# Optimization experiments

Measured on AMD Instinct MI355X. Metric: run time of the kernel, lower is better.

## Reference

```python
import jax, jax.numpy as jnp
import numpy as np


def _conv(x, w, b):
    # PyTorch Conv2d(k=4, s=2, p=1): NCHW x OIHW correlation
    y = jax.lax.conv_general_dilated(x, w, window_strides=(2, 2),
                                     padding=((1, 1), (1, 1)),
                                     dimension_numbers=('NCHW', 'OIHW', 'NCHW'))
    return y + b[None, :, None, None]


def _conv_t(x, w, b):
    # PyTorch ConvTranspose2d(k=4, s=2, p=1); w has torch shape (Cin, Cout, 4, 4).
    # Adjoint of strided correlation = correlation with spatially-flipped,
    # channel-swapped kernel and lhs dilation; pad = k - 1 - p = 2.
    wk = jnp.flip(w, (2, 3)).transpose(1, 0, 2, 3)  # (Cout, Cin, 4, 4)
    y = jax.lax.conv_general_dilated(x, wk, window_strides=(1, 1),
                                     padding=((2, 2), (2, 2)),
                                     lhs_dilation=(2, 2),
                                     dimension_numbers=('NCHW', 'OIHW', 'NCHW'))
    return y + b[None, :, None, None]


def setup_inputs() -> dict:
    key = jax.random.key(0)
    ks = jax.random.split(key, 18)
    s = 0.05
    inp = {'x': jax.random.normal(ks[0], (32, 3, 256, 256), jnp.float32)}
    # encoder weights (OIHW)
    enc_shapes = [(64, 3, 4, 4), (128, 64, 4, 4), (256, 128, 4, 4), (512, 256, 4, 4)]
    for i, sh in enumerate(enc_shapes):
        inp[f'e_w{i+1}'] = jax.random.normal(ks[1 + i], sh, jnp.float32) * s
        inp[f'e_b{i+1}'] = jnp.zeros((sh[0],), jnp.float32)
    # decoder weights (torch ConvTranspose2d layout: Cin, Cout, kH, kW)
    dec_shapes = [(512, 128, 4, 4), (128, 64, 4, 4), (64, 32, 4, 4), (32, 3, 4, 4)]
    for i, sh in enumerate(dec_shapes):
        inp[f'd_w{i+1}'] = jax.random.normal(ks[5 + i], sh, jnp.float32) * s
        inp[f'd_b{i+1}'] = jnp.zeros((sh[1],), jnp.float32)
    # codebook (num_embeddings=1024, embedding_dim=512)
    inp['embed'] = jax.random.normal(ks[9], (1024, 512), jnp.float32)
    return inp


def reference(x, e_w1, e_b1, e_w2, e_b2, e_w3, e_b3, e_w4, e_b4,
              d_w1, d_b1, d_w2, d_b2, d_w3, d_b3, d_w4, d_b4, embed):
    # encoder
    h = jax.nn.relu(_conv(x, e_w1, e_b1))
    h = jax.nn.relu(_conv(h, e_w2, e_b2))
    h = jax.nn.relu(_conv(h, e_w3, e_b3))
    z = jax.nn.relu(_conv(h, e_w4, e_b4))  # (B, 512, 16, 16)
    # quantizer: NCHW -> NHWC -> flat (B*H*W, D)
    B, D, H, W = z.shape
    z_flat = z.transpose(0, 2, 3, 1).reshape(-1, D)
    # squared L2 distance to each code: ||z||^2 - 2 z.E^T + ||E||^2
    dist = (jnp.sum(z_flat ** 2, axis=1, keepdims=True)
            - 2.0 * z_flat @ embed.T
            + jnp.sum(embed ** 2, axis=1))  # (N, K)
    idx = jnp.argmin(dist, axis=1)
    quantized = embed[idx]  # gather == one_hot @ embed
    z_q = quantized.reshape(B, H, W, D).transpose(0, 3, 1, 2)  # NCHW
    # decoder
    h = jax.nn.relu(_conv_t(z_q, d_w1, d_b1))
    h = jax.nn.relu(_conv_t(h, d_w2, d_b2))
    h = jax.nn.relu(_conv_t(h, d_w3, d_b3))
    out = jnp.tanh(_conv_t(h, d_w4, d_b4))  # (B, 3, 256, 256)
    return out
```

## Files before the change

kernel.cpp:

```cpp
#include <hip/hip_runtime.h>
#include <math.h>


typedef __attribute__((ext_vector_type(8))) short bf16x8;
typedef __attribute__((ext_vector_type(4))) float f32x4;
union FragU { unsigned u[4]; bf16x8 v; };

__device__ __forceinline__ unsigned bf16_rne(unsigned u) {
    return (u + 0x7FFFu + ((u >> 16) & 1u)) >> 16;
}
__device__ __forceinline__ unsigned pack_split(float v) {
    unsigned u = __builtin_bit_cast(unsigned, v);
    unsigned hi = bf16_rne(u);
    float hif = __builtin_bit_cast(float, hi << 16);
    float r = v - hif;
    unsigned lo = bf16_rne(__builtin_bit_cast(unsigned, r));
    return hi | (lo << 16);
}

__global__ void __launch_bounds__(256) pack_tensor(
    const float* __restrict__ s, unsigned* __restrict__ d, int n)
{
    int i = blockIdx.x * 256 + threadIdx.x;
    if (i < n) d[i] = pack_split(s[i]);
}

__global__ void __launch_bounds__(256) pack_w1(
    const float* __restrict__ w, unsigned* __restrict__ wq)
{
    int idx = blockIdx.x * 256 + threadIdx.x;
    if (idx >= 64 * 64) return;
    int k = idx & 63, oc = idx >> 6;
    float v = (k < 48) ? w[oc * 48 + k] : 0.0f;
    wq[idx] = pack_split(v);
}

template<int Cin, int Cout>
__global__ void __launch_bounds__(256) repack_wt(
    const float* __restrict__ w, unsigned* __restrict__ wq)
{
    constexpr int TOT = 16 * Cin * Cout;
    int idx = blockIdx.x * 256 + threadIdx.x;
    if (idx >= TOT) return;
    int t  = idx & 3;
    int ci = (idx >> 2) % Cin;
    int rest = (idx >> 2) / Cin;
    int co  = rest % Cout;
    int par = rest / Cout;
    int dy = par >> 1, dx = par & 1;
    int r = t >> 1, s = t & 1;
    int ky = 3 - dy - 2 * r;
    int kx = 3 - dx - 2 * s;
    float v = w[(((size_t)ci * Cout + co) * 4 + ky) * 4 + kx];
    wq[idx] = pack_split(v);
}

__global__ void __launch_bounds__(256) embed_transpose(
    const float* __restrict__ embed, float* __restrict__ et)
{
    int idx = blockIdx.x * 256 + threadIdx.x;
    int c = idx & 1023, k = idx >> 10;
    et[idx] = embed[(size_t)c * 512 + k];
}

template<int Cin, int H, int W, int Cout, int NB, int PACKO>
__global__ void __launch_bounds__(256) conv4s2_mfma(
    const unsigned* __restrict__ xp, const unsigned* __restrict__ wp,
    const float* __restrict__ bias, float* __restrict__ y)
{
    constexpr int OH = H / 2, OW = W / 2;
    constexpr int LOG_OW = (OW == 64) ? 6 : (OW == 32) ? 5 : 4;
    constexpr int R   = 64 / OW;
    constexpr int RT  = 2 * R + 2;
    constexpr int CS  = W + 2;
    constexpr int XEL = 2 * RT * CS;
    constexpr int XIT = (XEL + 255) / 256;
    constexpr int K   = Cin * 16;
    constexpr int NC  = Cin / 2;
    constexpr int NT  = NB / 64;
    constexpr int WIT = NB / 8;
    constexpr int MBC = 32 * OH * OW / 64;
    constexpr int XPAD = (XEL + 7) & ~7;
    constexpr int SM1 = XPAD + NB * 36;
    constexpr int SM2 = NB * 68;
    constexpr int SMEM = SM1 > SM2 ? SM1 : SM2;

    __shared__ unsigned smem[SMEM];
    unsigned* raw = smem;
    unsigned* wb  = smem + XPAD;

    int bid = blockIdx.x;
    int mb = bid % MBC, ng = bid / MBC;
    int oc0 = ng * NB;
    int m0 = mb * 64;
    int nimg = m0 / (OH * OW);
    int sp0 = m0 % (OH * OW);
    int oyb = sp0 >> LOG_OW;

    int tid  = threadIdx.x;
    int lane = tid & 63, wv = tid >> 6;
    int lm = lane & 15, q = lane >> 4;
    int n0w = wv * 16 * NT;

    const unsigned* xbase = xp + (size_t)nimg * Cin * H * W;

    int  goff[XIT];
    bool gok[XIT];
#pragma unroll
    for (int s = 0; s < XIT; ++s) {
        int i = tid + 256 * s;
        goff[s] = 0; gok[s] = false;
        if (i < XEL) {
            int lc = i % CS;
            int t2 = i / CS;
            int lr = t2 % RT;
            int c  = t2 / RT;
            int gr = 2 * oyb - 1 + lr;
            int gc = lc - 1;
            bool ok = ((unsigned)gr < (unsigned)H) && ((unsigned)gc < (unsigned)W);
            goff[s] = ok ? (c * H * W + gr * W + gc) : 0;
            gok[s]  = ok;
        }
    }
    const unsigned* wbase = wp + (size_t)(oc0 + (tid >> 5)) * K + (tid & 31);
    int wlds0 = (tid >> 5) * 36 + (tid & 31);

    f32x4 acc[4][NT];
#pragma unroll
    for (int nt = 0; nt < NT; ++nt) {
        float b = bias[oc0 + n0w + nt * 16 + lm];
#pragma unroll
        for (int mt = 0; mt < 4; ++mt)
#pragma unroll
            for (int r = 0; r < 4; ++r) acc[mt][nt][r] = b;
    }

    unsigned pfa[XIT];
    unsigned pfb[WIT];

    auto load_chunk = [&](int ch) {
        const unsigned* cb = xbase + (size_t)(ch * 2) * (H * W);
#pragma unroll
        for (int s = 0; s < XIT; ++s) {
            unsigned v = 0;
            if (gok[s]) v = cb[goff[s]];
            pfa[s] = v;
        }
        const unsigned* wc = wbase + ch * 32;
#pragma unroll
        for (int s = 0; s < WIT; ++s) pfb[s] = wc[(size_t)s * 8 * K];
    };
    auto store_chunk = [&]() {
#pragma unroll
        for (int s = 0; s < XIT; ++s) {
            int i = tid + 256 * s;
            if (i < XEL) raw[i] = pfa[s];
        }
#pragma unroll
        for (int s = 0; s < WIT; ++s) wb[wlds0 + s * 288] = pfb[s];
    };

    load_chunk(0);
#pragma unroll 1
    for (int ch = 0; ch < NC; ++ch) {
        __syncthreads();
        store_chunk();
        __syncthreads();
        if (ch + 1 < NC) load_chunk(ch + 1);

        FragU bhi[NT], blo[NT];
#pragma unroll
        for (int nt = 0; nt < NT; ++nt) {
            const unsigned* bp = &wb[(n0w + nt * 16 + lm) * 36 + q * 8];
            uint4 p0 = *(const uint4*)bp;
            uint4 p1 = *(const uint4*)(bp + 4);
            unsigned e0 = p0.x, e1 = p0.y, e2 = p0.z, e3 = p0.w;
            unsigned e4 = p1.x, e5 = p1.y, e6 = p1.z, e7 = p1.w;
            bhi[nt].u[0] = (e0 & 0xffffu) | (e1 << 16);
            bhi[nt].u[1] = (e2 & 0xffffu) | (e3 << 16);
            bhi[nt].u[2] = (e4 & 0xffffu) | (e5 << 16);
            bhi[nt].u[3] = (e6 & 0xffffu) | (e7 << 16);
            blo[nt].u[0] = (e0 >> 16) | (e1 & 0xffff0000u);
            blo[nt].u[1] = (e2 >> 16) | (e3 & 0xffff0000u);
            blo[nt].u[2] = (e4 >> 16) | (e5 & 0xffff0000u);
            blo[nt].u[3] = (e6 >> 16) | (e7 & 0xffff0000u);
        }
#pragma unroll
        for (int mt = 0; mt < 4; ++mt) {
            int m = mt * 16 + lm;
            int oyl = m >> LOG_OW, oxl = m & (OW - 1);
            int c = q >> 1, rb = 2 * oyl + (q & 1) * 2;
            const unsigned* rp = &raw[(c * RT + rb) * CS + 2 * oxl];
            uint2 a0 = *(const uint2*)rp;
            uint2 a1 = *(const uint2*)(rp + 2);
            uint2 a2 = *(const uint2*)(rp + CS);
            uint2 a3 = *(const uint2*)(rp + CS + 2);
            FragU ahi, alo;
            ahi.u[0] = (a0.x & 0xffffu) | (a0.y << 16);
            ahi.u[1] = (a1.x & 0xffffu) | (a1.y << 16);
            ahi.u[2] = (a2.x & 0xffffu) | (a2.y << 16);
            ahi.u[3] = (a3.x & 0xffffu) | (a3.y << 16);
            alo.u[0] = (a0.x >> 16) | (a0.y & 0xffff0000u);
            alo.u[1] = (a1.x >> 16) | (a1.y & 0xffff0000u);
            alo.u[2] = (a2.x >> 16) | (a2.y & 0xffff0000u);
            alo.u[3] = (a3.x >> 16) | (a3.y & 0xffff0000u);
#pragma unroll
            for (int nt = 0; nt < NT; ++nt) {
                acc[mt][nt] = __builtin_amdgcn_mfma_f32_16x16x32_bf16(
                    ahi.v, bhi[nt].v, acc[mt][nt], 0, 0, 0);
                acc[mt][nt] = __builtin_amdgcn_mfma_f32_16x16x32_bf16(
                    ahi.v, blo[nt].v, acc[mt][nt], 0, 0, 0);
                acc[mt][nt] = __builtin_amdgcn_mfma_f32_16x16x32_bf16(
                    alo.v, bhi[nt].v, acc[mt][nt], 0, 0, 0);
            }
        }
    }

    __syncthreads();
    float* cs = (float*)smem;
#pragma unroll
    for (int mt = 0; mt < 4; ++mt)
#pragma unroll
        for (int nt = 0; nt < NT; ++nt) {
            int nl = n0w + nt * 16 + lm;
#pragma unroll
            for (int r = 0; r < 4; ++r)
                cs[nl * 68 + mt * 16 + q * 4 + r] = acc[mt][nt][r];
        }
    __syncthreads();
    {
        constexpr int QT = 256 / NB;
        constexpr int MQ = 64 / QT;
        int nl = tid / QT, qt = tid % QT;
        size_t gb = ((size_t)(nimg * Cout + oc0 + nl)) * (OH * OW) + sp0 + qt * MQ;
#pragma unroll
        for (int i2 = 0; i2 < MQ / 4; ++i2) {
            float4 v = *(float4*)&cs[nl * 68 + qt * MQ + 4 * i2];
            v.x = fmaxf(v.x, 0.0f); v.y = fmaxf(v.y, 0.0f);
            v.z = fmaxf(v.z, 0.0f); v.w = fmaxf(v.w, 0.0f);
            if (PACKO) {
                uint4 p;
                p.x = pack_split(v.x); p.y = pack_split(v.y);
                p.z = pack_split(v.z); p.w = pack_split(v.w);
                *(uint4*)((unsigned*)y + gb + 4 * i2) = p;
            } else {
                *(float4*)(y + gb + 4 * i2) = v;
            }
        }
    }
}

template<int Cin, int CINR, int H, int W, int Cout, int MT, int NT, int PACKO>
__global__ void __launch_bounds__(256) conv4s2_mfma_g(
    const unsigned* __restrict__ xp, const unsigned* __restrict__ wp,
    const float* __restrict__ bias, float* __restrict__ y)
{
    constexpr int OH = H / 2, OW = W / 2;
    constexpr int OWB = (OW >= 64) ? 64 : OW;
    constexpr int LOG_OWB = (OWB == 64) ? 6 : (OWB == 32) ? 5 : 4;
    constexpr int LOG_OW  = (OW == 128) ? 7 : (OW == 64) ? 6 : (OW == 32) ? 5 : 4;
    constexpr int R   = 64 / OWB;
    constexpr int RT  = 2 * R + 2;
    constexpr int CS  = 2 * OWB + 2;
    constexpr int XEL = 2 * RT * CS;
    constexpr int XIT = (XEL + 255) / 256;
    constexpr int K   = Cin * 16;
    constexpr int NC  = Cin / 2;
    constexpr int NB  = Cout;
    constexpr int WIT = NB / 8;
    constexpr int WN  = Cout / (16 * NT);
    constexpr int WM  = 4 / WN;
    static_assert(WM * MT * 16 == 64, "M tiling");
    static_assert(WN * NT * 16 == Cout, "N tiling");
    constexpr int MBC = 32 * OH * OW / 64;
    constexpr int XPAD = (XEL + 7) & ~7;
    constexpr int SM1 = XPAD + NB * 36;
    constexpr int SM2 = NB * 68;
    constexpr int SMEM = SM1 > SM2 ? SM1 : SM2;

    __shared__ unsigned smem[SMEM];
    unsigned* raw = smem;
    unsigned* wb  = smem + XPAD;

    int bid = blockIdx.x;
    int mb = bid % MBC, ng = bid / MBC;
    int oc0 = ng * NB;
    int m0 = bid % MBC * 64;
    m0 = mb * 64;
    int nimg = m0 / (OH * OW);
    int sp0 = m0 % (OH * OW);
    int oyb = sp0 >> LOG_OW;
    int oxb = sp0 & (OW - 1);

    int tid  = threadIdx.x;
    int lane = tid & 63, wv = tid >> 6;
    int lm = lane & 15, q = lane >> 4;
    int wm = wv / WN, wn = wv % WN;

    const unsigned* xbase = xp + (size_t)nimg * CINR * H * W;

    int  goff[XIT];
    bool gok[XIT];
    int  cidx[XIT];
#pragma unroll
    for (int s = 0; s < XIT; ++s) {
        int i = tid + 256 * s;
        goff[s] = 0; gok[s] = false; cidx[s] = 0;
        if (i < XEL) {
            int lc = i % CS;
            int t2 = i / CS;
            int lr = t2 % RT;
            int c  = t2 / RT;
            int gr = 2 * oyb - 1 + lr;
            int gc = 2 * oxb - 1 + lc;
            bool ok = ((unsigned)gr < (unsigned)H) && ((unsigned)gc < (unsigned)W);
            goff[s] = ok ? (c * H * W + gr * W + gc) : 0;
            gok[s]  = ok;
            cidx[s] = c;
        }
    }
    const unsigned* wbase = wp + (size_t)(oc0 + (tid >> 5)) * K + (tid & 31);
    int wlds0 = (tid >> 5) * 36 + (tid & 31);

    f32x4 acc[MT][NT];
#pragma unroll
    for (int nt = 0; nt < NT; ++nt) {
        float b = bias[oc0 + wn * NT * 16 + nt * 16 + lm];
#pragma unroll
        for (int mt = 0; mt < MT; ++mt)
#pragma unroll
            for (int r = 0; r < 4; ++r) acc[mt][nt][r] = b;
    }

    unsigned pfa[XIT];
    unsigned pfb[WIT];

    auto load_chunk = [&](int ch) {
        const unsigned* cb = xbase + (size_t)(ch * 2) * (H * W);
#pragma unroll
        for (int s = 0; s < XIT; ++s) {
            unsigned v = 0;
            bool okc = (2 * ch + cidx[s]) < CINR;
            if (gok[s] && okc) v = cb[goff[s]];
            pfa[s] = v;
        }
        const unsigned* wc = wbase + ch * 32;
#pragma unroll
        for (int s = 0; s < WIT; ++s) pfb[s] = wc[(size_t)s * 8 * K];
    };
    auto store_chunk = [&]() {
#pragma unroll
        for (int s = 0; s < XIT; ++s) {
            int i = tid + 256 * s;
            if (i < XEL) raw[i] = pfa[s];
        }
#pragma unroll
        for (int s = 0; s < WIT; ++s) wb[wlds0 + s * 288] = pfb[s];
    };

    load_chunk(0);
#pragma unroll 1
    for (int ch = 0; ch < NC; ++ch) {
        __syncthreads();
        store_chunk();
        __syncthreads();
        if (ch + 1 < NC) load_chunk(ch + 1);

        FragU bhi[NT], blo[NT];
#pragma unroll
        for (int nt = 0; nt < NT; ++nt) {
            const unsigned* bp = &wb[(wn * NT * 16 + nt * 16 + lm) * 36 + q * 8];
            uint4 p0 = *(const uint4*)bp;
            uint4 p1 = *(const uint4*)(bp + 4);
            unsigned e0 = p0.x, e1 = p0.y, e2 = p0.z, e3 = p0.w;
            unsigned e4 = p1.x, e5 = p1.y, e6 = p1.z, e7 = p1.w;
            bhi[nt].u[0] = (e0 & 0xffffu) | (e1 << 16);
            bhi[nt].u[1] = (e2 & 0xffffu) | (e3 << 16);
            bhi[nt].u[2] = (e4 & 0xffffu) | (e5 << 16);
            bhi[nt].u[3] = (e6 & 0xffffu) | (e7 << 16);
            blo[nt].u[0] = (e0 >> 16) | (e1 & 0xffff0000u);
            blo[nt].u[1] = (e2 >> 16) | (e3 & 0xffff0000u);
            blo[nt].u[2] = (e4 >> 16) | (e5 & 0xffff0000u);
            blo[nt].u[3] = (e6 >> 16) | (e7 & 0xffff0000u);
        }
#pragma unroll
        for (int mt = 0; mt < MT; ++mt) {
            int m = wm * (MT * 16) + mt * 16 + lm;
            int oyl = m >> LOG_OWB, oxl = m & (OWB - 1);
            int c = q >> 1, rb = 2 * oyl + (q & 1) * 2;
            const unsigned* rp = &raw[(c * RT + rb) * CS + 2 * oxl];
            uint2 a0 = *(const uint2*)rp;
            uint2 a1 = *(const uint2*)(rp + 2);
            uint2 a2 = *(const uint2*)(rp + CS);
            uint2 a3 = *(const uint2*)(rp + CS + 2);
            FragU ahi, alo;
            ahi.u[0] = (a0.x & 0xffffu) | (a0.y << 16);
            ahi.u[1] = (a1.x & 0xffffu) | (a1.y << 16);
            ahi.u[2] = (a2.x & 0xffffu) | (a2.y << 16);
            ahi.u[3] = (a3.x & 0xffffu) | (a3.y << 16);
            alo.u[0] = (a0.x >> 16) | (a0.y & 0xffff0000u);
            alo.u[1] = (a1.x >> 16) | (a1.y & 0xffff0000u);
            alo.u[2] = (a2.x >> 16) | (a2.y & 0xffff0000u);
            alo.u[3] = (a3.x >> 16) | (a3.y & 0xffff0000u);
#pragma unroll
            for (int nt = 0; nt < NT; ++nt) {
                acc[mt][nt] = __builtin_amdgcn_mfma_f32_16x16x32_bf16(
                    ahi.v, bhi[nt].v, acc[mt][nt], 0, 0, 0);
                acc[mt][nt] = __builtin_amdgcn_mfma_f32_16x16x32_bf16(
                    ahi.v, blo[nt].v, acc[mt][nt], 0, 0, 0);
                acc[mt][nt] = __builtin_amdgcn_mfma_f32_16x16x32_bf16(
                    alo.v, bhi[nt].v, acc[mt][nt], 0, 0, 0);
            }
        }
    }

    __syncthreads();
    float* cs = (float*)smem;
#pragma unroll
    for (int mt = 0; mt < MT; ++mt)
#pragma unroll
        for (int nt = 0; nt < NT; ++nt) {
            int nl  = wn * NT * 16 + nt * 16 + lm;
            int mb2 = wm * (MT * 16) + mt * 16 + q * 4;
#pragma unroll
            for (int r = 0; r < 4; ++r)
                cs[nl * 68 + mb2 + r] = acc[mt][nt][r];
        }
    __syncthreads();
    {
        constexpr int QT = 256 / NB;
        constexpr int MQ = 64 / QT;
        int nl = tid / QT, qt = tid % QT;
        size_t gb = ((size_t)(nimg * Cout + oc0 + nl)) * (OH * OW) + sp0 + qt * MQ;
#pragma unroll
        for (int i2 = 0; i2 < MQ / 4; ++i2) {
            float4 v = *(float4*)&cs[nl * 68 + qt * MQ + 4 * i2];
            v.x = fmaxf(v.x, 0.0f); v.y = fmaxf(v.y, 0.0f);
            v.z = fmaxf(v.z, 0.0f); v.w = fmaxf(v.w, 0.0f);
            if (PACKO) {
                uint4 p;
                p.x = pack_split(v.x); p.y = pack_split(v.y);
                p.z = pack_split(v.z); p.w = pack_split(v.w);
                *(uint4*)((unsigned*)y + gb + 4 * i2) = p;
            } else {
                *(float4*)(y + gb + 4 * i2) = v;
            }
        }
    }
}

template<int Cin, int Hh, int Wh, int Cout, int MT, int NT, int PACKO>
__global__ void __launch_bounds__(256) convt4s2_mfma(
    const unsigned* __restrict__ xp, const unsigned* __restrict__ wq,
    const float* __restrict__ bias, float* __restrict__ y)
{
    constexpr int W = Wh;
    constexpr int LOG_W = (W == 64) ? 6 : (W == 32) ? 5 : 4;
    constexpr int R   = 64 / W;
    constexpr int RT  = R + 1;
    constexpr int CS  = W + 2;
    constexpr int XEL = 8 * RT * CS;
    constexpr int XIT = (XEL + 255) / 256;
    constexpr int K   = Cin * 4;
    constexpr int NC  = Cin / 8;
    constexpr int NB  = Cout;
    constexpr int WIT = NB / 8;
    constexpr int WN  = Cout / (16 * NT);
    constexpr int WM  = 4 / WN;
    static_assert(WM * MT * 16 == 64, "M tiling");
    static_assert(WN * NT * 16 == Cout, "N tiling");
    constexpr int MBC = 32 * Hh * W / 64;
    constexpr int XPAD = (XEL + 7) & ~7;
    constexpr int SM1 = XPAD + NB * 36;
    constexpr int SM2 = NB * 68;
    constexpr int SMEM = SM1 > SM2 ? SM1 : SM2;

    __shared__ unsigned smem[SMEM];
    unsigned* raw = smem;
    unsigned* wb  = smem + XPAD;

    int bid = blockIdx.x;
    int mb  = bid % MBC;
    int par = bid / MBC;
    int dy = par >> 1, dx = par & 1;

    int m0   = mb * 64;
    int nimg = m0 / (Hh * W);
    int sp0  = m0 % (Hh * W);
    int il0  = sp0 >> LOG_W;

    int tid = threadIdx.x;
    int lane = tid & 63, wv = tid >> 6;
    int lm = lane & 15, q = lane >> 4;
    int wm = wv / WN, wn = wv % WN;

    const unsigned* xbase = xp + (size_t)nimg * Cin * Hh * W;

    int  goff[XIT];
    bool gok[XIT];
#pragma unroll
    for (int s = 0; s < XIT; ++s) {
        int i = tid + 256 * s;
        goff[s] = 0; gok[s] = false;
        if (i < XEL) {
            int lc = i % CS;
            int t2 = i / CS;
            int lr = t2 % RT;
            int c  = t2 / RT;
            int gr = il0 - 1 + dy + lr;
            int gc = lc - 1;
            bool ok = ((unsigned)gr < (unsigned)Hh) && ((unsigned)gc < (unsigned)W);
            goff[s] = ok ? (c * Hh * W + gr * W + gc) : 0;
            gok[s]  = ok;
        }
    }
    const unsigned* wbase = wq + (size_t)(par * Cout + (tid >> 5)) * K + (tid & 31);
    int wlds0 = (tid >> 5) * 36 + (tid & 31);

    f32x4 acc[MT][NT];
#pragma unroll
    for (int nt = 0; nt < NT; ++nt) {
        float b = bias[wn * NT * 16 + nt * 16 + lm];
#pragma unroll
        for (int mt = 0; mt < MT; ++mt)
#pragma unroll
            for (int r = 0; r < 4; ++r) acc[mt][nt][r] = b;
    }

    unsigned pfa[XIT];
    unsigned pfb[WIT];

    auto load_chunk = [&](int ch) {
        const unsigned* cb = xbase + (size_t)(ch * 8) * (Hh * W);
#pragma unroll
        for (int s = 0; s < XIT; ++s) {
            unsigned v = 0;
            if (gok[s]) v = cb[goff[s]];
            pfa[s] = v;
        }
        const unsigned* wc = wbase + ch * 32;
#pragma unroll
        for (int s = 0; s < WIT; ++s) pfb[s] = wc[(size_t)s * 8 * K];
    };
    auto store_chunk = [&]() {
#pragma unroll
        for (int s = 0; s < XIT; ++s) {
            int i = tid + 256 * s;
            if (i < XEL) raw[i] = pfa[s];
        }
#pragma unroll
        for (int s = 0; s < WIT; ++s) wb[wlds0 + s * 288] = pfb[s];
    };

    load_chunk(0);
#pragma unroll 1
    for (int ch = 0; ch < NC; ++ch) {
        __syncthreads();
        store_chunk();
        __syncthreads();
        if (ch + 1 < NC) load_chunk(ch + 1);

        FragU bhi[NT], blo[NT];
#pragma unroll
        for (int nt = 0; nt < NT; ++nt) {
            const unsigned* bp = &wb[(wn * NT * 16 + nt * 16 + lm) * 36 + q * 8];
            uint4 p0 = *(const uint4*)bp;
            uint4 p1 = *(const uint4*)(bp + 4);
            unsigned e0 = p0.x, e1 = p0.y, e2 = p0.z, e3 = p0.w;
            unsigned e4 = p1.x, e5 = p1.y, e6 = p1.z, e7 = p1.w;
            bhi[nt].u[0] = (e0 & 0xffffu) | (e1 << 16);
            bhi[nt].u[1] = (e2 & 0xffffu) | (e3 << 16);
            bhi[nt].u[2] = (e4 & 0xffffu) | (e5 << 16);
            bhi[nt].u[3] = (e6 & 0xffffu) | (e7 << 16);
            blo[nt].u[0] = (e0 >> 16) | (e1 & 0xffff0000u);
            blo[nt].u[1] = (e2 >> 16) | (e3 & 0xffff0000u);
            blo[nt].u[2] = (e4 >> 16) | (e5 & 0xffff0000u);
            blo[nt].u[3] = (e6 >> 16) | (e7 & 0xffff0000u);
        }
#pragma unroll
        for (int mt = 0; mt < MT; ++mt) {
            int ml = wm * (MT * 16) + mt * 16 + lm;
            int il = ml >> LOG_W, jl = ml & (W - 1);
            const unsigned* rp = &raw[((2 * q) * RT + il) * CS + jl + dx];
            unsigned a00 = rp[0],               a01 = rp[1];
            unsigned a10 = rp[CS],              a11 = rp[CS + 1];
            unsigned a20 = rp[RT * CS],         a21 = rp[RT * CS + 1];
            unsigned a30 = rp[RT * CS + CS],    a31 = rp[RT * CS + CS + 1];
            FragU ahi, alo;
            ahi.u[0] = (a00 & 0xffffu) | (a01 << 16);
            ahi.u[1] = (a10 & 0xffffu) | (a11 << 16);
            ahi.u[2] = (a20 & 0xffffu) | (a21 << 16);
            ahi.u[3] = (a30 & 0xffffu) | (a31 << 16);
            alo.u[0] = (a00 >> 16) | (a01 & 0xffff0000u);
            alo.u[1] = (a10 >> 16) | (a11 & 0xffff0000u);
            alo.u[2] = (a20 >> 16) | (a21 & 0xffff0000u);
            alo.u[3] = (a30 >> 16) | (a31 & 0xffff0000u);
#pragma unroll
            for (int nt = 0; nt < NT; ++nt) {
                acc[mt][nt] = __builtin_amdgcn_mfma_f32_16x16x32_bf16(
                    ahi.v, bhi[nt].v, acc[mt][nt], 0, 0, 0);
                acc[mt][nt] = __builtin_amdgcn_mfma_f32_16x16x32_bf16(
                    ahi.v, blo[nt].v, acc[mt][nt], 0, 0, 0);
                acc[mt][nt] = __builtin_amdgcn_mfma_f32_16x16x32_bf16(
                    alo.v, bhi[nt].v, acc[mt][nt], 0, 0, 0);
            }
        }
    }

    __syncthreads();
    float* cs = (float*)smem;
#pragma unroll
    for (int mt = 0; mt < MT; ++mt)
#pragma unroll
        for (int nt = 0; nt < NT; ++nt) {
            int nl  = wn * NT * 16 + nt * 16 + lm;
            int mb2 = wm * (MT * 16) + mt * 16 + q * 4;
#pragma unroll
            for (int r = 0; r < 4; ++r)
                cs[nl * 68 + mb2 + r] = acc[mt][nt][r];
        }
    __syncthreads();
    constexpr int EIT = NB * 64 / 256;
#pragma unroll
    for (int it = 0; it < EIT; ++it) {
        int idx = tid + 256 * it;
        int c = idx >> 6, m = idx & 63;
        int il = m >> LOG_W, jl = m & (W - 1);
        int oy = 2 * (il0 + il) + dy;
        int ox = 2 * jl + dx;
        float v = fmaxf(cs[c * 68 + m], 0.0f);
        size_t go = (((size_t)(nimg * Cout + c)) * (2 * Hh) + oy) * (2 * W) + ox;
        if (PACKO) ((unsigned*)y)[go] = pack_split(v);
        else       y[go] = v;
    }
}

template<int Cin, int H, int W, int Cout, int COT, int ACT, int UNR>
__global__ void __launch_bounds__(256) convt4s2_k(
    const float* __restrict__ x, const float* __restrict__ w,
    const float* __restrict__ bias, float* __restrict__ y)
{
    constexpr int OH = 2 * H, OW = 2 * W, OWq = OW / 4;
    int id = blockIdx.x * 256 + threadIdx.x;
    int ox4 = id % OWq; int t = id / OWq;
    int oy  = t % OH;   t /= OH;
    int cog = t % (Cout / COT);
    int n   = t / (Cout / COT);
    int co0 = __builtin_amdgcn_readfirstlane(cog * COT);
    n       = __builtin_amdgcn_readfirstlane(n);

    int p   = (oy + 1) & 1;
    int iyA = (oy + 1 - p) >> 1;
    int iyB = iyA - 1;
    bool vA = (iyA < H);
    bool vB = (iyB >= 0);
    int iyAc = vA ? iyA : 0, iyBc = vB ? iyB : 0;

    int t0 = 2 * ox4;
    bool c0 = (t0 - 1 >= 0);
    bool c3 = (t0 + 2 <= W - 1);
    int j0 = c0 ? t0 - 1 : 0;
    int j3 = c3 ? t0 + 2 : 0;

    float acc[COT][4];
#pragma unroll
    for (int o = 0; o < COT; ++o) {
        float b = bias[co0 + o];
#pragma unroll
        for (int j = 0; j < 4; ++j) acc[o][j] = b;
    }

    const float* xn = x + (size_t)n * Cin * H * W;

#pragma unroll UNR
    for (int ci = 0; ci < Cin; ++ci) {
        const float* xc  = xn + (size_t)ci * (H * W);
        const float* xrA = xc + (size_t)iyAc * W;
        const float* xrB = xc + (size_t)iyBc * W;
        float a0 = (vA && c0) ? xrA[j0]     : 0.0f;
        float a1 =  vA        ? xrA[t0]     : 0.0f;
        float a2 =  vA        ? xrA[t0 + 1] : 0.0f;
        float a3 = (vA && c3) ? xrA[j3]     : 0.0f;
        float b0 = (vB && c0) ? xrB[j0]     : 0.0f;
        float b1 =  vB        ? xrB[t0]     : 0.0f;
        float b2 =  vB        ? xrB[t0 + 1] : 0.0f;
        float b3 = (vB && c3) ? xrB[j3]     : 0.0f;

        const float* wci = w + ((size_t)ci * Cout + co0) * 16;
#pragma unroll
        for (int o = 0; o < COT; ++o) {
            const float* wr = wci + (size_t)o * 16;
            float wA0 = wr[p * 4 + 0], wA1 = wr[p * 4 + 1];
            float wA2 = wr[p * 4 + 2], wA3 = wr[p * 4 + 3];
            float wB0 = wr[(p + 2) * 4 + 0], wB1 = wr[(p + 2) * 4 + 1];
            float wB2 = wr[(p + 2) * 4 + 2], wB3 = wr[(p + 2) * 4 + 3];
            acc[o][0] = fmaf(a1, wA1, acc[o][0]); acc[o][0] = fmaf(a0, wA3, acc[o][0]);
            acc[o][0] = fmaf(b1, wB1, acc[o][0]); acc[o][0] = fmaf(b0, wB3, acc[o][0]);
            acc[o][1] = fmaf(a2, wA0, acc[o][1]); acc[o][1] = fmaf(a1, wA2, acc[o][1]);
            acc[o][1] = fmaf(b2, wB0, acc[o][1]); acc[o][1] = fmaf(b1, wB2, acc[o][1]);
            acc[o][2] = fmaf(a2, wA1, acc[o][2]); acc[o][2] = fmaf(a1, wA3, acc[o][2]);
            acc[o][2] = fmaf(b2, wB1, acc[o][2]); acc[o][2] = fmaf(b1, wB3, acc[o][2]);
            acc[o][3] = fmaf(a3, wA0, acc[o][3]); acc[o][3] = fmaf(a2, wA2, acc[o][3]);
            acc[o][3] = fmaf(b3, wB0, acc[o][3]); acc[o][3] = fmaf(b2, wB2, acc[o][3]);
        }
    }

    int ox0 = ox4 * 4;
#pragma unroll
    for (int o = 0; o < COT; ++o) {
        float* yr = y + (((size_t)n * Cout + co0 + o) * OH + oy) * OW + ox0;
#pragma unroll
        for (int j = 0; j < 4; ++j) {
            float v = acc[o][j];
            yr[j] = (ACT == 0) ? fmaxf(v, 0.0f) : tanhf(v);
        }
    }
}

__global__ void __launch_bounds__(256) embed_norms(
    const float* __restrict__ embed, float* __restrict__ norms)
{
    int c = blockIdx.x * 256 + threadIdx.x;
    const float* e = embed + (size_t)c * 512;
    float s = 0.0f;
    for (int k = 0; k < 512; ++k) s = fmaf(e[k], e[k], s);
    norms[c] = s;
}

__global__ void __launch_bounds__(256, 4) vq_argmin8v(
    const float* __restrict__ z, const float* __restrict__ et,
    const float* __restrict__ norms, int* __restrict__ out)
{
    constexpr int ZS = 516;
    int row0 = blockIdx.x * 8;
    int n    = row0 >> 8;
    int yx0  = row0 & 255;
    int tid  = threadIdx.x;

    __shared__ float zr[8 * ZS];

    const float* zn = z + ((size_t)n * 512) * 256;
#pragma unroll
    for (int it = 0; it < 4; ++it) {
        int i  = tid + 256 * it;
        int rq = i & 1, kc = i >> 1;
        float4 v = *(const float4*)&zn[(size_t)kc * 256 + yx0 + 4 * rq];
        zr[(4 * rq + 0) * ZS + kc] = v.x;
        zr[(4 * rq + 1) * ZS + kc] = v.y;
        zr[(4 * rq + 2) * ZS + kc] = v.z;
        zr[(4 * rq + 3) * ZS + kc] = v.w;
    }
    __syncthreads();

    f32x4 acc[8];
#pragma unroll
    for (int r = 0; r < 8; ++r) acc[r] = (f32x4){0.f, 0.f, 0.f, 0.f};

    const float* ebase = et + 4 * tid;
    f32x4 ev[4], fv[4];
#pragma unroll
    for (int j = 0; j < 4; ++j)
        ev[j] = *(const f32x4*)&ebase[(size_t)j * 1024];

#pragma unroll 1
    for (int k4 = 0; k4 < 128; ++k4) {
        int kn = (k4 + 1 < 128) ? k4 + 1 : 127;
#pragma unroll
        for (int j = 0; j < 4; ++j)
            fv[j] = *(const f32x4*)&ebase[(size_t)(4 * kn + j) * 1024];
#pragma unroll
        for (int r = 0; r < 8; ++r) {
            float4 zz = *(const float4*)&zr[r * ZS + 4 * k4];
            f32x4 a = acc[r];
            a += ev[0] * zz.x;
            a += ev[1] * zz.y;
            a += ev[2] * zz.z;
            a += ev[3] * zz.w;
            acc[r] = a;
        }
#pragma unroll
        for (int j = 0; j < 4; ++j) ev[j] = fv[j];
    }

    float4 nb = *(const float4*)&norms[4 * tid];
    float best[8]; int bi[8];
#pragma unroll
    for (int r = 0; r < 8; ++r) {
        float d0 = nb.x - 2.0f * acc[r][0];
        float d1 = nb.y - 2.0f * acc[r][1];
        float d2 = nb.z - 2.0f * acc[r][2];
        float d3 = nb.w - 2.0f * acc[r][3];
        float b = d0; int ix = 4 * tid;
        if (d1 < b) { b = d1; ix = 4 * tid + 1; }
        if (d2 < b) { b = d2; ix = 4 * tid + 2; }
        if (d3 < b) { b = d3; ix = 4 * tid + 3; }
        best[r] = b; bi[r] = ix;
    }

    __syncthreads();
    float* rbd = zr;
    int*   rbi = (int*)(zr + 2048);
#pragma unroll
    for (int r = 0; r < 8; ++r) {
        rbd[r * 256 + tid] = best[r];
        rbi[r * 256 + tid] = bi[r];
    }
    __syncthreads();
    for (int s = 128; s > 0; s >>= 1) {
        if (tid < s) {
#pragma unroll
            for (int r = 0; r < 8; ++r) {
                int i0 = r * 256 + tid;
                float od = rbd[i0 + s]; int oi = rbi[i0 + s];
                float md = rbd[i0];     int mi = rbi[i0];
                if (od < md || (od == md && oi < mi)) { rbd[i0] = od; rbi[i0] = oi; }
            }
        }
        __syncthreads();
    }
    if (tid < 8) out[row0 + tid] = rbi[tid * 256];
}

__global__ void __launch_bounds__(256) vq_gather_pack(
    const int* __restrict__ vidx, const float* __restrict__ embed,
    unsigned* __restrict__ zq)
{
    int i = blockIdx.x * 256 + threadIdx.x;
    int yx = i & 255;
    int t  = i >> 8;
    int c  = t & 511;
    int n  = t >> 9;
    int row = (n << 8) + yx;
    zq[i] = pack_split(embed[(size_t)vidx[row] * 512 + c]);
}

extern "C" void kernel_launch(void* const* d_in, const int* in_sizes, int n_in,
                              void* d_out, int out_size, void* d_ws, size_t ws_size,
                              hipStream_t stream)
{
    (void)in_sizes; (void)n_in; (void)out_size; (void)ws_size;
    const float* x     = (const float*)d_in[0];
    const float* ew1   = (const float*)d_in[1];
    const float* eb1   = (const float*)d_in[2];
    const float* ew2   = (const float*)d_in[3];
    const float* eb2   = (const float*)d_in[4];
    const float* ew3   = (const float*)d_in[5];
    const float* eb3   = (const float*)d_in[6];
    const float* ew4   = (const float*)d_in[7];
    const float* eb4   = (const float*)d_in[8];
    const float* dw1   = (const float*)d_in[9];
    const float* db1   = (const float*)d_in[10];
    const float* dw2   = (const float*)d_in[11];
    const float* db2   = (const float*)d_in[12];
    const float* dw3   = (const float*)d_in[13];
    const float* db3   = (const float*)d_in[14];
    const float* dw4   = (const float*)d_in[15];
    const float* db4   = (const float*)d_in[16];
    const float* embed = (const float*)d_in[17];
    float* out = (float*)d_out;

    unsigned* W0   = (unsigned*)d_ws;
    unsigned* h1p  = W0;
    unsigned* h2p  = W0 + 33554432;
    unsigned* xp1  = W0 + 33554432;
    unsigned* h3p  = W0;
    float*    z    = (float*)(W0 + 8388608);
    unsigned* zq   = W0 + 12582912;
    float*    P0   = (float*)(W0 + 16777216);
    float*    P1   = (float*)(W0 + 20971520);
    int*      vidx = (int*)(W0 + 29360128);
    float*    norms= (float*)(W0 + 29368320);
    float*    g3o  = (float*)h2p;

    unsigned* wp2 = (unsigned*)d_out;
    unsigned* wp3 = wp2 + 131072;
    unsigned* wp4 = wp2 + 655360;
    unsigned* wq1 = wp2 + 2752512;
    unsigned* wq2 = wq1 + 1048576;
    unsigned* wq3 = wq2 + 131072;
    float*    et  = (float*)(wq3 + 32768);
    unsigned* wp1 = (unsigned*)(et + 524288);

    dim3 b256(256);

    pack_tensor<<<dim3(512),  b256, 0, stream>>>(ew2, wp2, 131072);
    pack_tensor<<<dim3(2048), b256, 0, stream>>>(ew3, wp3, 524288);
    pack_tensor<<<dim3(8192), b256, 0, stream>>>(ew4, wp4, 2097152);
    pack_w1<<<dim3(16), b256, 0, stream>>>(ew1, wp1);
    pack_tensor<<<dim3(24576), b256, 0, stream>>>(x, xp1, 6291456);
    repack_wt<512, 128><<<dim3(4096), b256, 0, stream>>>(dw1, wq1);
    repack_wt<128,  64><<<dim3(512),  b256, 0, stream>>>(dw2, wq2);
    repack_wt< 64,  32><<<dim3(128),  b256, 0, stream>>>(dw3, wq3);
    embed_transpose<<<dim3(2048), b256, 0, stream>>>(embed, et);

    conv4s2_mfma_g<4, 3, 256, 256, 64, 4, 1, 1><<<dim3(8192), b256, 0, stream>>>(
        xp1, wp1, eb1, (float*)h1p);
    conv4s2_mfma<64, 128, 128, 128, 128, 1><<<dim3(2048), b256, 0, stream>>>(
        h1p, wp2, eb2, (float*)h2p);
    conv4s2_mfma<128, 64, 64, 256, 128, 1><<<dim3(1024), b256, 0, stream>>>(
        h2p, wp3, eb3, (float*)h3p);
    conv4s2_mfma<256, 32, 32, 512, 64, 0><<<dim3(1024), b256, 0, stream>>>(
        h3p, wp4, eb4, z);

    embed_norms<<<dim3(4), b256, 0, stream>>>(embed, norms);
    vq_argmin8v<<<dim3(1024), b256, 0, stream>>>(z, et, norms, vidx);
    vq_gather_pack<<<dim3(16384), b256, 0, stream>>>(vidx, embed, zq);

    convt4s2_mfma<512, 16, 16, 128, 4, 2, 1><<<dim3(4 * 128), b256, 0, stream>>>(
        zq, wq1, db1, P0);
    convt4s2_mfma<128, 32, 32, 64, 4, 1, 1><<<dim3(4 * 512), b256, 0, stream>>>(
        (const unsigned*)P0, wq2, db2, P1);
    convt4s2_mfma<64, 64, 64, 32, 2, 1, 0><<<dim3(4 * 2048), b256, 0, stream>>>(
        (const unsigned*)P1, wq3, db3, g3o);
    convt4s2_k<32, 128, 128, 3, 3, 1, 2><<<dim3(2048), b256, 0, stream>>>(
        g3o, dw4, db4, out);
}
```

Before: 1.132 ms.

## Pre-split weights into hi/lo bf16 planes and stage activation fragments in LDS

Weight packing now produces separate hi and lo bf16 planes, so the conv and transposed-conv kernels load MFMA B fragments directly with vector LDS reads instead of unpacking them per wave. Activations are also cooperatively converted once per chunk into hi/lo fragment tiles in LDS, so they are not re-gathered and re-split for every output-channel tile. This removes repeated bit-manipulation ALU work and strided LDS reads from the inner loop. In exchange it adds an extra LDS pass and an extra __syncthreads per chunk, plus more shared memory.

```diff
diff --git a/kernel.cpp b/kernel.cpp
--- a/kernel.cpp
+++ b/kernel.cpp
@@ -35,24 +35,51 @@
     wq[idx] = pack_split(v);
 }
 
-template<int Cin, int Cout>
-__global__ void __launch_bounds__(256) repack_wt(
+template<int Cout, int K>
+__global__ void __launch_bounds__(256) pack_w_planes(
     const float* __restrict__ w, unsigned* __restrict__ wq)
 {
-    constexpr int TOT = 16 * Cin * Cout;
+    constexpr int K2 = K / 2;
+    constexpr int TOT = Cout * K;
     int idx = blockIdx.x * 256 + threadIdx.x;
     if (idx >= TOT) return;
-    int t  = idx & 3;
-    int ci = (idx >> 2) % Cin;
-    int rest = (idx >> 2) / Cin;
-    int co  = rest % Cout;
-    int par = rest / Cout;
+    int kp   = idx % K2;
+    int rest = idx / K2;
+    int oc   = rest % Cout;
+    int p    = rest / Cout;
+    unsigned u0 = pack_split(w[(size_t)oc * K + 2 * kp]);
+    unsigned u1 = pack_split(w[(size_t)oc * K + 2 * kp + 1]);
+    wq[idx] = (p == 0) ? ((u0 & 0xffffu) | (u1 << 16))
+                       : ((u0 >> 16) | (u1 & 0xffff0000u));
+}
+
+template<int Cin, int Cout>
+__global__ void __launch_bounds__(256) repack_wt_planes(
+    const float* __restrict__ w, unsigned* __restrict__ wq)
+{
+    constexpr int K = Cin * 4, K2 = K / 2;
+    constexpr int TOT = 2 * 4 * Cout * K2;
+    int idx = blockIdx.x * 256 + threadIdx.x;
+    if (idx >= TOT) return;
+    int kp   = idx % K2;
+    int rest = idx / K2;
+    int co   = rest % Cout;
+    rest    /= Cout;
+    int par  = rest & 3;
+    int p    = rest >> 2;
     int dy = par >> 1, dx = par & 1;
-    int r = t >> 1, s = t & 1;
-    int ky = 3 - dy - 2 * r;
-    int kx = 3 - dx - 2 * s;
-    float v = w[(((size_t)ci * Cout + co) * 4 + ky) * 4 + kx];
-    wq[idx] = pack_split(v);
+    unsigned u01[2];
+#pragma unroll
+    for (int e = 0; e < 2; ++e) {
+        int k = 2 * kp + e;
+        int t = k & 3, ci = k >> 2;
+        int r = t >> 1, s = t & 1;
+        int ky = 3 - dy - 2 * r;
+        int kx = 3 - dx - 2 * s;
+        u01[e] = pack_split(w[(((size_t)ci * Cout + co) * 4 + ky) * 4 + kx]);
+    }
+    wq[idx] = (p == 0) ? ((u01[0] & 0xffffu) | (u01[1] << 16))
+                       : ((u01[0] >> 16) | (u01[1] & 0xffff0000u));
 }
 
 __global__ void __launch_bounds__(256) embed_transpose(
@@ -76,18 +103,27 @@
     constexpr int XEL = 2 * RT * CS;
     constexpr int XIT = (XEL + 255) / 256;
     constexpr int K   = Cin * 16;
+    constexpr int K2  = K / 2;
     constexpr int NC  = Cin / 2;
     constexpr int NT  = NB / 64;
+    constexpr int WR  = NB / 16;
     constexpr int WIT = NB / 8;
     constexpr int MBC = 32 * OH * OW / 64;
     constexpr int XPAD = (XEL + 7) & ~7;
-    constexpr int SM1 = XPAD + NB * 36;
+    constexpr int OFF_WH = XPAD;
+    constexpr int OFF_WL = OFF_WH + NB * 20;
+    constexpr int OFF_AH = OFF_WL + NB * 20;
+    constexpr int OFF_AL = OFF_AH + 64 * 20;
+    constexpr int SM1 = OFF_AL + 64 * 20;
     constexpr int SM2 = NB * 68;
     constexpr int SMEM = SM1 > SM2 ? SM1 : SM2;
 
     __shared__ unsigned smem[SMEM];
     unsigned* raw = smem;
-    unsigned* wb  = smem + XPAD;
+    unsigned* wbh = smem + OFF_WH;
+    unsigned* wbl = smem + OFF_WL;
+    unsigned* afh = smem + OFF_AH;
+    unsigned* afl = smem + OFF_AL;
 
     int bid = blockIdx.x;
     int mb = bid % MBC, ng = bid / MBC;
@@ -122,8 +158,9 @@
             gok[s]  = ok;
         }
     }
-    const unsigned* wbase = wp + (size_t)(oc0 + (tid >> 5)) * K + (tid & 31);
-    int wlds0 = (tid >> 5) * 36 + (tid & 31);
+    const unsigned* wbase_h = wp + (size_t)(oc0 + (tid >> 4)) * K2 + (tid & 15);
+    const unsigned* wbase_l = wbase_h + (size_t)Cout * K2;
+    int wlds0 = (tid >> 4) * 20 + (tid & 15);
 
     f32x4 acc[4][NT];
 #pragma unroll
@@ -146,9 +183,13 @@
             if (gok[s]) v = cb[goff[s]];
             pfa[s] = v;
         }
-        const unsigned* wc = wbase + ch * 32;
-#pragma unroll
-        for (int s = 0; s < WIT; ++s) pfb[s] = wc[(size_t)s * 8 * K];
+        const unsigned* wch = wbase_h + ch * 16;
+        const unsigned* wcl = wbase_l + ch * 16;
+#pragma unroll
+        for (int s = 0; s < WR; ++s) {
+            pfb[2 * s]     = wch[(size_t)s * 16 * K2];
+            pfb[2 * s + 1] = wcl[(size_t)s * 16 * K2];
+        }
     };
     auto store_chunk = [&]() {
 #pragma unroll
@@ -157,7 +198,10 @@
             if (i < XEL) raw[i] = pfa[s];
         }
 #pragma unroll
-        for (int s = 0; s < WIT; ++s) wb[wlds0 + s * 288] = pfb[s];
+        for (int s = 0; s < WR; ++s) {
+            wbh[wlds0 + s * 16 * 20] = pfb[2 * s];
+            wbl[wlds0 + s * 16 * 20] = pfb[2 * s + 1];
+        }
     };
 
     load_chunk(0);
@@ -166,44 +210,39 @@
         __syncthreads();
         store_chunk();
         __syncthreads();
+#pragma unroll
+        for (int t = 0; t < 4; ++t) {
+            int job = tid + 256 * t;
+            int m = job & 63, kp = job >> 6;
+            int oyl = m >> LOG_OW, oxl = m & (OW - 1);
+            int c = kp >> 3, ky = (kp >> 1) & 3, kxp = kp & 1;
+            int ro = (c * RT + 2 * oyl + ky) * CS + 2 * oxl + 2 * kxp;
+            unsigned r0 = raw[ro], r1 = raw[ro + 1];
+            afh[m * 20 + kp] = (r0 & 0xffffu) | (r1 << 16);
+            afl[m * 20 + kp] = (r0 >> 16) | (r1 & 0xffff0000u);
+        }
         if (ch + 1 < NC) load_chunk(ch + 1);
+        __syncthreads();
 
         FragU bhi[NT], blo[NT];
 #pragma unroll
         for (int nt = 0; nt < NT; ++nt) {
-            const unsigned* bp = &wb[(n0w + nt * 16 + lm) * 36 + q * 8];
-            uint4 p0 = *(const uint4*)bp;
-            uint4 p1 = *(const uint4*)(bp + 4);
-            unsigned e0 = p0.x, e1 = p0.y, e2 = p0.z, e3 = p0.w;
-            unsigned e4 = p1.x, e5 = p1.y, e6 = p1.z, e7 = p1.w;
-            bhi[nt].u[0] = (e0 & 0xffffu) | (e1 << 16);
-            bhi[nt].u[1] = (e2 & 0xffffu) | (e3 << 16);
-            bhi[nt].u[2] = (e4 & 0xffffu) | (e5 << 16);
-            bhi[nt].u[3] = (e6 & 0xffffu) | (e7 << 16);
-            blo[nt].u[0] = (e0 >> 16) | (e1 & 0xffff0000u);
-            blo[nt].u[1] = (e2 >> 16) | (e3 & 0xffff0000u);
-            blo[nt].u[2] = (e4 >> 16) | (e5 & 0xffff0000u);
-            blo[nt].u[3] = (e6 >> 16) | (e7 & 0xffff0000u);
+            int oc = n0w + nt * 16 + lm;
+            uint4 th = *(const uint4*)&wbh[oc * 20 + q * 4];
+            uint4 tl = *(const uint4*)&wbl[oc * 20 + q * 4];
+            bhi[nt].u[0] = th.x; bhi[nt].u[1] = th.y;
+            bhi[nt].u[2] = th.z; bhi[nt].u[3] = th.w;
+            blo[nt].u[0] = tl.x; blo[nt].u[1] = tl.y;
+            blo[nt].u[2] = tl.z; blo[nt].u[3] = tl.w;
         }
 #pragma unroll
         for (int mt = 0; mt < 4; ++mt) {
             int m = mt * 16 + lm;
-            int oyl = m >> LOG_OW, oxl = m & (OW - 1);
-            int c = q >> 1, rb = 2 * oyl + (q & 1) * 2;
-            const unsigned* rp = &raw[(c * RT + rb) * CS + 2 * oxl];
-            uint2 a0 = *(const uint2*)rp;
-            uint2 a1 = *(const uint2*)(rp + 2);
-            uint2 a2 = *(const uint2*)(rp + CS);
-            uint2 a3 = *(const uint2*)(rp + CS + 2);
+            uint4 ah = *(const uint4*)&afh[m * 20 + q * 4];
+            uint4 al = *(const uint4*)&afl[m * 20 + q * 4];
             FragU ahi, alo;
-            ahi.u[0] = (a0.x & 0xffffu) | (a0.y << 16);
-            ahi.u[1] = (a1.x & 0xffffu) | (a1.y << 16);
-            ahi.u[2] = (a2.x & 0xffffu) | (a2.y << 16);
-            ahi.u[3] = (a3.x & 0xffffu) | (a3.y << 16);
-            alo.u[0] = (a0.x >> 16) | (a0.y & 0xffff0000u);
-            alo.u[1] = (a1.x >> 16) | (a1.y & 0xffff0000u);
-            alo.u[2] = (a2.x >> 16) | (a2.y & 0xffff0000u);
-            alo.u[3] = (a3.x >> 16) | (a3.y & 0xffff0000u);
+            ahi.u[0] = ah.x; ahi.u[1] = ah.y; ahi.u[2] = ah.z; ahi.u[3] = ah.w;
+            alo.u[0] = al.x; alo.u[1] = al.y; alo.u[2] = al.z; alo.u[3] = al.w;
 #pragma unroll
             for (int nt = 0; nt < NT; ++nt) {
                 acc[mt][nt] = __builtin_amdgcn_mfma_f32_16x16x32_bf16(
@@ -285,8 +324,7 @@
     int bid = blockIdx.x;
     int mb = bid % MBC, ng = bid / MBC;
     int oc0 = ng * NB;
-    int m0 = bid % MBC * 64;
-    m0 = mb * 64;
+    int m0 = mb * 64;
     int nimg = m0 / (OH * OW);
     int sp0 = m0 % (OH * OW);
     int oyb = sp0 >> LOG_OW;
@@ -462,8 +500,10 @@
     constexpr int XEL = 8 * RT * CS;
     constexpr int XIT = (XEL + 255) / 256;
     constexpr int K   = Cin * 4;
+    constexpr int K2  = K / 2;
     constexpr int NC  = Cin / 8;
     constexpr int NB  = Cout;
+    constexpr int WR  = NB / 16;
     constexpr int WIT = NB / 8;
     constexpr int WN  = Cout / (16 * NT);
     constexpr int WM  = 4 / WN;
@@ -471,13 +511,20 @@
     static_assert(WN * NT * 16 == Cout, "N tiling");
     constexpr int MBC = 32 * Hh * W / 64;
     constexpr int XPAD = (XEL + 7) & ~7;
-    constexpr int SM1 = XPAD + NB * 36;
+    constexpr int OFF_WH = XPAD;
+    constexpr int OFF_WL = OFF_WH + NB * 20;
+    constexpr int OFF_AH = OFF_WL + NB * 20;
+    constexpr int OFF_AL = OFF_AH + 64 * 20;
+    constexpr int SM1 = OFF_AL + 64 * 20;
     constexpr int SM2 = NB * 68;
     constexpr int SMEM = SM1 > SM2 ? SM1 : SM2;
 
     __shared__ unsigned smem[SMEM];
     unsigned* raw = smem;
-    unsigned* wb  = smem + XPAD;
+    unsigned* wbh = smem + OFF_WH;
+    unsigned* wbl = smem + OFF_WL;
+    unsigned* afh = smem + OFF_AH;
+    unsigned* afl = smem + OFF_AL;
 
     int bid = blockIdx.x;
     int mb  = bid % MBC;
@@ -514,8 +561,9 @@
             gok[s]  = ok;
         }
     }
-    const unsigned* wbase = wq + (size_t)(par * Cout + (tid >> 5)) * K + (tid & 31);
-    int wlds0 = (tid >> 5) * 36 + (tid & 31);
+    const unsigned* wbase_h = wq + (size_t)(par * Cout + (tid >> 4)) * K2 + (tid & 15);
+    const unsigned* wbase_l = wbase_h + (size_t)4 * Cout * K2;
+    int wlds0 = (tid >> 4) * 20 + (tid & 15);
 
     f32x4 acc[MT][NT];
 #pragma unroll
@@ -538,9 +586,13 @@
             if (gok[s]) v = cb[goff[s]];
             pfa[s] = v;
         }
-        const unsigned* wc = wbase + ch * 32;
-#pragma unroll
-        for (int s = 0; s < WIT; ++s) pfb[s] = wc[(size_t)s * 8 * K];
+        const unsigned* wch = wbase_h + ch * 16;
+        const unsigned* wcl = wbase_l + ch * 16;
+#pragma unroll
+        for (int s = 0; s < WR; ++s) {
+            pfb[2 * s]     = wch[(size_t)s * 16 * K2];
+            pfb[2 * s + 1] = wcl[(size_t)s * 16 * K2];
+        }
     };
     auto store_chunk = [&]() {
 #pragma unroll
@@ -549,7 +601,10 @@
             if (i < XEL) raw[i] = pfa[s];
         }
 #pragma unroll
-        for (int s = 0; s < WIT; ++s) wb[wlds0 + s * 288] = pfb[s];
+        for (int s = 0; s < WR; ++s) {
+            wbh[wlds0 + s * 16 * 20] = pfb[2 * s];
+            wbl[wlds0 + s * 16 * 20] = pfb[2 * s + 1];
+        }
     };
 
     load_chunk(0);
@@ -558,43 +613,39 @@
         __syncthreads();
         store_chunk();
         __syncthreads();
+#pragma unroll
+        for (int t = 0; t < 4; ++t) {
+            int job = tid + 256 * t;
+            int m = job & 63, kp = job >> 6;
+            int il = m >> LOG_W, jl = m & (W - 1);
+            int cl = kp >> 1, r = kp & 1;
+            int ro = (cl * RT + il + r) * CS + jl + dx;
+            unsigned r0 = raw[ro], r1 = raw[ro + 1];
+            afh[m * 20 + kp] = (r0 & 0xffffu) | (r1 << 16);
+            afl[m * 20 + kp] = (r0 >> 16) | (r1 & 0xffff0000u);
+        }
         if (ch + 1 < NC) load_chunk(ch + 1);
+        __syncthreads();
 
         FragU bhi[NT], blo[NT];
 #pragma unroll
         for (int nt = 0; nt < NT; ++nt) {
-            const unsigned* bp = &wb[(wn * NT * 16 + nt * 16 + lm) * 36 + q * 8];
-            uint4 p0 = *(const uint4*)bp;
-            uint4 p1 = *(const uint4*)(bp + 4);
-            unsigned e0 = p0.x, e1 = p0.y, e2 = p0.z, e3 = p0.w;
-            unsigned e4 = p1.x, e5 = p1.y, e6 = p1.z, e7 = p1.w;
-            bhi[nt].u[0] = (e0 & 0xffffu) | (e1 << 16);
-            bhi[nt].u[1] = (e2 & 0xffffu) | (e3 << 16);
-            bhi[nt].u[2] = (e4 & 0xffffu) | (e5 << 16);
-            bhi[nt].u[3] = (e6 & 0xffffu) | (e7 << 16);
-            blo[nt].u[0] = (e0 >> 16) | (e1 & 0xffff0000u);
-            blo[nt].u[1] = (e2 >> 16) | (e3 & 0xffff0000u);
-            blo[nt].u[2] = (e4 >> 16) | (e5 & 0xffff0000u);
-            blo[nt].u[3] = (e6 >> 16) | (e7 & 0xffff0000u);
+            int oc = wn * NT * 16 + nt * 16 + lm;
+            uint4 th = *(const uint4*)&wbh[oc * 20 + q * 4];
+            uint4 tl = *(const uint4*)&wbl[oc * 20 + q * 4];
+            bhi[nt].u[0] = th.x; bhi[nt].u[1] = th.y;
+            bhi[nt].u[2] = th.z; bhi[nt].u[3] = th.w;
+            blo[nt].u[0] = tl.x; blo[nt].u[1] = tl.y;
+            blo[nt].u[2] = tl.z; blo[nt].u[3] = tl.w;
         }
 #pragma unroll
         for (int mt = 0; mt < MT; ++mt) {
             int ml = wm * (MT * 16) + mt * 16 + lm;
-            int il = ml >> LOG_W, jl = ml & (W - 1);
-            const unsigned* rp = &raw[((2 * q) * RT + il) * CS + jl + dx];
-            unsigned a00 = rp[0],               a01 = rp[1];
-            unsigned a10 = rp[CS],              a11 = rp[CS + 1];
-            unsigned a20 = rp[RT * CS],         a21 = rp[RT * CS + 1];
-            unsigned a30 = rp[RT * CS + CS],    a31 = rp[RT * CS + CS + 1];
+            uint4 ah = *(const uint4*)&afh[ml * 20 + q * 4];
+            uint4 al = *(const uint4*)&afl[ml * 20 + q * 4];
             FragU ahi, alo;
-            ahi.u[0] = (a00 & 0xffffu) | (a01 << 16);
-            ahi.u[1] = (a10 & 0xffffu) | (a11 << 16);
-            ahi.u[2] = (a20 & 0xffffu) | (a21 << 16);
-            ahi.u[3] = (a30 & 0xffffu) | (a31 << 16);
-            alo.u[0] = (a00 >> 16) | (a01 & 0xffff0000u);
-            alo.u[1] = (a10 >> 16) | (a11 & 0xffff0000u);
-            alo.u[2] = (a20 >> 16) | (a21 & 0xffff0000u);
-            alo.u[3] = (a30 >> 16) | (a31 & 0xffff0000u);
+            ahi.u[0] = ah.x; ahi.u[1] = ah.y; ahi.u[2] = ah.z; ahi.u[3] = ah.w;
+            alo.u[0] = al.x; alo.u[1] = al.y; alo.u[2] = al.z; alo.u[3] = al.w;
 #pragma unroll
             for (int nt = 0; nt < NT; ++nt) {
                 acc[mt][nt] = __builtin_amdgcn_mfma_f32_16x16x32_bf16(
@@ -883,14 +934,14 @@
 
     dim3 b256(256);
 
-    pack_tensor<<<dim3(512),  b256, 0, stream>>>(ew2, wp2, 131072);
-    pack_tensor<<<dim3(2048), b256, 0, stream>>>(ew3, wp3, 524288);
-    pack_tensor<<<dim3(8192), b256, 0, stream>>>(ew4, wp4, 2097152);
+    pack_w_planes<128, 1024><<<dim3(512),  b256, 0, stream>>>(ew2, wp2);
+    pack_w_planes<256, 2048><<<dim3(2048), b256, 0, stream>>>(ew3, wp3);
+    pack_w_planes<512, 4096><<<dim3(8192), b256, 0, stream>>>(ew4, wp4);
     pack_w1<<<dim3(16), b256, 0, stream>>>(ew1, wp1);
     pack_tensor<<<dim3(24576), b256, 0, stream>>>(x, xp1, 6291456);
-    repack_wt<512, 128><<<dim3(4096), b256, 0, stream>>>(dw1, wq1);
-    repack_wt<128,  64><<<dim3(512),  b256, 0, stream>>>(dw2, wq2);
-    repack_wt< 64,  32><<<dim3(128),  b256, 0, stream>>>(dw3, wq3);
+    repack_wt_planes<512, 128><<<dim3(4096), b256, 0, stream>>>(dw1, wq1);
+    repack_wt_planes<128,  64><<<dim3(512),  b256, 0, stream>>>(dw2, wq2);
+    repack_wt_planes< 64,  32><<<dim3(128),  b256, 0, stream>>>(dw3, wq3);
     embed_transpose<<<dim3(2048), b256, 0, stream>>>(embed, et);
 
     conv4s2_mfma_g<4, 3, 256, 256, 64, 4, 1, 1><<<dim3(8192), b256, 0, stream>>>(
```

After: 1.180 ms. 1.04x slower.
